# Kernel tuning notes

Hardware: AMD Instinct MI355X
Metric: run time of the kernel (lower is better)

## Reference

```python
import jax, jax.numpy as jnp
import numpy as np

V, C, L, D = 50000, 125000, 500000, 128


def _l2norm(x):
    n = jnp.sqrt(jnp.sum(x * x, axis=-1, keepdims=True))
    return x / jnp.maximum(n, 1e-12)


def _combine(x, W1, b1, W2, b2):
    # SymmetricSumCombine element op: normalize(sigmoid(layer1(x)) + layer2(x));
    # the outer sum over set members is done by segment_sum by the caller.
    return _l2norm(jax.nn.sigmoid(x @ W1 + b1) + (x @ W2 + b2))


def setup_inputs() -> dict:
    key = jax.random.key(0)
    ks = jax.random.split(key, 22)
    s = 1.0 / np.sqrt(D)
    w = lambda k: jax.random.normal(k, (D, D), jnp.float32) * s
    b = lambda k: jax.random.normal(k, (D,), jnp.float32) * s
    return {
        "variables": jax.random.normal(ks[0], (V, D), jnp.float32),
        "lit_var": jax.random.randint(ks[1], (L,), 0, V, jnp.int32),
        "lit_sign": jax.random.randint(ks[2], (L,), 0, 2, jnp.int32),
        "lit_clause": jnp.sort(jax.random.randint(ks[3], (L,), 0, C, jnp.int32)),
        "clause_var": jax.random.randint(ks[4], (C,), 0, V, jnp.int32),
        "neg_W": w(ks[5]), "neg_b": b(ks[6]),
        "vc_W1": w(ks[7]), "vc_b1": b(ks[8]), "vc_W2": w(ks[9]), "vc_b2": b(ks[10]),
        "cc_W1": w(ks[11]), "cc_b1": b(ks[12]), "cc_W2": w(ks[13]), "cc_b2": b(ks[14]),
        "W_z": w(ks[15]), "U_z": w(ks[16]), "W_r": w(ks[17]), "U_r": w(ks[18]),
        "W_h": w(ks[19]), "U_h": w(ks[20]),
    }


def reference(variables, lit_var, lit_sign, lit_clause, clause_var,
              neg_W, neg_b, vc_W1, vc_b1, vc_W2, vc_b2,
              cc_W1, cc_b1, cc_W2, cc_b2,
              W_z, U_z, W_r, U_r, W_h, U_h):
    n_vars = variables.shape[0]
    n_clauses = clause_var.shape[0]
    # gather per-literal variable embeddings, negate negative literals
    v = variables[lit_var]  # [L, D]
    v = jnp.where((lit_sign > 0)[:, None], v @ neg_W + neg_b, v)
    # variable_combiner per literal, summed into clause embeddings
    t = _combine(v, vc_W1, vc_b1, vc_W2, vc_b2)  # [L, D]
    ce = jax.ops.segment_sum(t, lit_clause, num_segments=n_clauses)  # [C, D]
    # clause_combiner per clause, summed into owner variable message
    c = _combine(ce, cc_W1, cc_b1, cc_W2, cc_b2)  # [C, D]
    av = jax.ops.segment_sum(c, clause_var, num_segments=n_vars)  # [V, D]
    # variables with no clauses keep their own embedding as the message
    cnt = jnp.zeros((n_vars,), jnp.float32).at[clause_var].add(1.0)
    av = jnp.where((cnt > 0)[:, None], av, variables)
    # GRU update
    z = jax.nn.sigmoid(av @ W_z + variables @ U_z)
    r = jax.nn.sigmoid(av @ W_r + variables @ U_r)
    h_tilda = jnp.tanh(av @ W_h + (r * variables) @ U_h)
    return (1.0 - z) * variables + z * h_tilda
```

## Files before the change

### kernel.cpp

```cpp
#include <hip/hip_runtime.h>

#define V_N 50000
#define C_N 125000
#define L_N 500000
#define NCH2 31250

typedef __attribute__((ext_vector_type(8))) short short8;
typedef __attribute__((ext_vector_type(4))) float f32x4;

__device__ inline unsigned short f2bf(float f) {
  union { float f; unsigned u; } v; v.f = f;
  unsigned r = v.u + 0x7FFFu + ((v.u >> 16) & 1u);
  return (unsigned short)(r >> 16);
}
__device__ inline float bf2f(unsigned short h) {
  union { unsigned u; float f; } v; v.u = ((unsigned)h) << 16;
  return v.f;
}
__device__ inline float sigm(float x) { return 1.f / (1.f + __expf(-x)); }
__device__ inline unsigned packbf2(float a0, float a1) {
  return (unsigned)f2bf(a0) | ((unsigned)f2bf(a1) << 16);
}

struct WPtrs { const float* w[11]; };

__global__ __launch_bounds__(256) void k_front(
    WPtrs p, unsigned short* __restrict__ wt,
    const int* __restrict__ lit_var, const int* __restrict__ lit_sign,
    const int* __restrict__ lit_clause, int* __restrict__ pmeta,
    int* __restrict__ bnd, const int* __restrict__ clause_var,
    int* __restrict__ cnt, int* __restrict__ dst) {
  int b = blockIdx.x;
  if (b < 704) {
    int idx = b * 256 + threadIdx.x;
    int m = idx >> 14;
    int e14 = idx & 16383;
    int chunk = e14 >> 9;
    int rem = e14 & 511;
    int kq = rem >> 7;
    int lan15 = (rem >> 3) & 15;
    int e = rem & 7;
    int col = ((chunk >> 3) << 5) + (((chunk >> 2) & 1) << 4) + lan15;
    int k = ((chunk & 3) << 5) + (kq << 3) + e;
    wt[idx] = f2bf(p.w[m][k * 128 + col]);
  } else if (b < 2658) {
    int i = (b - 704) * 256 + threadIdx.x;
    if (i < L_N)
      pmeta[i] = lit_var[i] | (lit_sign[i] << 16) | ((lit_clause[i] & 63) << 17);
  } else if (b < 2781) {
    int i = (b - 2658) * 256 + threadIdx.x;
    if (i <= NCH2) {
      int key = i * 4;
      int lo = 0, hi = L_N;
      while (lo < hi) {
        int mid = (lo + hi) >> 1;
        if (lit_clause[mid] < key) lo = mid + 1; else hi = mid;
      }
      bnd[i] = lo;
    }
  } else {
    int i = (b - 2781) * 256 + threadIdx.x;
    if (i < C_N) {
      int v = clause_var[i];
      dst[i] = atomicAdd(&cnt[v], 1);
    }
  }
}

__device__ inline void load_bfrags(const unsigned short* __restrict__ Wt,
                                   short8 B[2][4], int wave, int lane) {
#pragma unroll
  for (int ct = 0; ct < 2; ++ct)
#pragma unroll
    for (int ks = 0; ks < 4; ++ks)
      B[ct][ks] = *(const short8*)(Wt + (((wave << 3) + (ct << 2) + ks) << 9) +
                                   (lane << 3));
}

__device__ inline void gemm_reg(const unsigned short (*__restrict__ xs)[136],
                                const short8 B[2][4], f32x4 acc[4][2], int lane) {
  const int lan15 = lane & 15, kq = lane >> 4;
#pragma unroll
  for (int ks = 0; ks < 4; ++ks) {
#pragma unroll
    for (int rt = 0; rt < 4; ++rt) {
      short8 a = *(const short8*)(&xs[rt * 16 + lan15][ks * 32 + kq * 8]);
#pragma unroll
      for (int ct = 0; ct < 2; ++ct)
        acc[rt][ct] = __builtin_amdgcn_mfma_f32_16x16x32_bf16(a, B[ct][ks], acc[rt][ct], 0, 0, 0);
    }
  }
}

__device__ inline void zero_acc(f32x4 acc[4][2]) {
#pragma unroll
  for (int rt = 0; rt < 4; ++rt)
#pragma unroll
    for (int ct = 0; ct < 2; ++ct) acc[rt][ct] = (f32x4)(0.f);
}

__device__ inline void gemm_reg32(const unsigned short (*__restrict__ xs)[136],
                                  const short8 B[2][4], f32x4 acc[2][2], int lane) {
  const int lan15 = lane & 15, kq = lane >> 4;
#pragma unroll
  for (int ks = 0; ks < 4; ++ks) {
#pragma unroll
    for (int rt = 0; rt < 2; ++rt) {
      short8 a = *(const short8*)(&xs[rt * 16 + lan15][ks * 32 + kq * 8]);
#pragma unroll
      for (int ct = 0; ct < 2; ++ct)
        acc[rt][ct] = __builtin_amdgcn_mfma_f32_16x16x32_bf16(a, B[ct][ks], acc[rt][ct], 0, 0, 0);
    }
  }
}

__device__ inline void zero_acc2(f32x4 acc[2][2]) {
#pragma unroll
  for (int rt = 0; rt < 2; ++rt)
#pragma unroll
    for (int ct = 0; ct < 2; ++ct) acc[rt][ct] = (f32x4)(0.f);
}

__device__ inline void stage_f32_32(const float* __restrict__ base, long vb, int nrows,
                                    unsigned short (*__restrict__ dst)[136], int tid) {
  int r = tid >> 3, cq = (tid & 7) * 16;
  long v = vb + r;
  bool valid = v < nrows;
  const float* src = valid ? base + v * 128 : base;
#pragma unroll
  for (int j = 0; j < 16; j += 4) {
    float4 x4 = *(const float4*)(src + cq + j);
    if (!valid) { x4.x = 0.f; x4.y = 0.f; x4.z = 0.f; x4.w = 0.f; }
    dst[r][cq + j + 0] = f2bf(x4.x);
    dst[r][cq + j + 1] = f2bf(x4.y);
    dst[r][cq + j + 2] = f2bf(x4.z);
    dst[r][cq + j + 3] = f2bf(x4.w);
  }
}

__global__ __launch_bounds__(256, 2) void k_tables(
    const float* __restrict__ vars,
    const unsigned short* __restrict__ negWt, const float* __restrict__ negb,
    const unsigned short* __restrict__ W1t, const float* __restrict__ b1,
    const unsigned short* __restrict__ W2t, const float* __restrict__ b2,
    unsigned short* __restrict__ t_pos, unsigned short* __restrict__ t_neg) {
  __shared__ unsigned short xs[32][136];
  __shared__ unsigned short ys[32][136];
  __shared__ float ssp[32][4];
  const int tid = threadIdx.x;
  const int wave = tid >> 6, lane = tid & 63;
  const int lan15 = lane & 15, kq = lane >> 4;
  const long vb = (long)blockIdx.x * 32;

  stage_f32_32(vars, vb, V_N, xs, tid);
  __syncthreads();

  float nb[2], bb1[2], bb2[2];
#pragma unroll
  for (int ct = 0; ct < 2; ++ct) {
    int col = wave * 32 + ct * 16 + lan15;
    nb[ct] = negb[col]; bb1[ct] = b1[col]; bb2[ct] = b2[col];
  }
  {
    short8 BN[2][4];
    load_bfrags(negWt, BN, wave, lane);
    f32x4 acc[2][2];
    zero_acc2(acc);
    gemm_reg32(xs, BN, acc, lane);
#pragma unroll
    for (int rt = 0; rt < 2; ++rt)
#pragma unroll
      for (int ct = 0; ct < 2; ++ct) {
        int col = wave * 32 + ct * 16 + lan15;
#pragma unroll
        for (int reg = 0; reg < 4; ++reg)
          ys[rt * 16 + kq * 4 + reg][col] = f2bf(acc[rt][ct][reg] + nb[ct]);
      }
  }
  __syncthreads();

  short8 B1f[2][4], B2f[2][4];
  load_bfrags(W1t, B1f, wave, lane);
  load_bfrags(W2t, B2f, wave, lane);

#pragma unroll
  for (int pass = 0; pass < 2; ++pass) {
    const unsigned short (*A)[136] = pass ? ys : xs;
    unsigned short* dst = pass ? t_neg : t_pos;
    f32x4 a1[2][2], a2[2][2];
    zero_acc2(a1); zero_acc2(a2);
    gemm_reg32(A, B1f, a1, lane);
    gemm_reg32(A, B2f, a2, lane);
    float s[2][2][4]; float ss[2][4];
#pragma unroll
    for (int rt = 0; rt < 2; ++rt) {
#pragma unroll
      for (int reg = 0; reg < 4; ++reg) ss[rt][reg] = 0.f;
#pragma unroll
      for (int ct = 0; ct < 2; ++ct)
#pragma unroll
        for (int reg = 0; reg < 4; ++reg) {
          float v = sigm(a1[rt][ct][reg] + bb1[ct]) + (a2[rt][ct][reg] + bb2[ct]);
          s[rt][ct][reg] = v; ss[rt][reg] += v * v;
        }
    }
#pragma unroll
    for (int rt = 0; rt < 2; ++rt)
#pragma unroll
      for (int reg = 0; reg < 4; ++reg) {
        float v = ss[rt][reg];
        v += __shfl_xor(v, 1); v += __shfl_xor(v, 2);
        v += __shfl_xor(v, 4); v += __shfl_xor(v, 8);
        if (lan15 == 0) ssp[rt * 16 + kq * 4 + reg][wave] = v;
      }
    __syncthreads();
#pragma unroll
    for (int rt = 0; rt < 2; ++rt)
#pragma unroll
      for (int reg = 0; reg < 4; ++reg) {
        int row = rt * 16 + kq * 4 + reg;
        float tot = ssp[row][0] + ssp[row][1] + ssp[row][2] + ssp[row][3];
        float inv = 1.f / fmaxf(sqrtf(tot), 1e-12f);
        long vr = vb + row;
        if (vr < V_N) {
#pragma unroll
          for (int ct = 0; ct < 2; ++ct)
            dst[vr * 128 + wave * 32 + ct * 16 + lan15] = f2bf(s[rt][ct][reg] * inv);
        }
      }
    __syncthreads();
  }
}

__global__ __launch_bounds__(256) void k_scan_pre(const int* __restrict__ cnt,
                                                  int* __restrict__ bsum) {
  __shared__ int sh[256];
  const int tid = threadIdx.x;
  int i = blockIdx.x * 256 + tid;
  int v = (i < V_N) ? cnt[i] : 0;
  sh[tid] = v;
  __syncthreads();
  for (int off = 1; off < 256; off <<= 1) {
    int add = (tid >= off) ? sh[tid - off] : 0;
    __syncthreads();
    sh[tid] += add;
    __syncthreads();
  }
  if (tid == 255) bsum[blockIdx.x] = sh[255];
}

__global__ __launch_bounds__(256) void k_scan_mid(int* __restrict__ bsum, int nb) {
  __shared__ int sh[256];
  const int tid = threadIdx.x;
  int v = (tid < nb) ? bsum[tid] : 0;
  sh[tid] = v;
  __syncthreads();
  for (int off = 1; off < 256; off <<= 1) {
    int add = (tid >= off) ? sh[tid - off] : 0;
    __syncthreads();
    sh[tid] += add;
    __syncthreads();
  }
  if (tid < nb) bsum[tid] = sh[tid] - v;
}

__global__ __launch_bounds__(256) void k_scan_post(const int* __restrict__ cnt,
                                                   const int* __restrict__ bsum,
                                                   int* __restrict__ col_start) {
  __shared__ int sh[256];
  const int tid = threadIdx.x;
  int i = blockIdx.x * 256 + tid;
  int v = (i < V_N) ? cnt[i] : 0;
  sh[tid] = v;
  __syncthreads();
  for (int off = 1; off < 256; off <<= 1) {
    int add = (tid >= off) ? sh[tid - off] : 0;
    __syncthreads();
    sh[tid] += add;
    __syncthreads();
  }
  if (i < V_N) col_start[i + 1] = sh[tid] + bsum[blockIdx.x];
  if (i == 0) col_start[0] = 0;
}

__global__ __launch_bounds__(256, 4) void k_sc_clause(
    const int* __restrict__ pmeta, const int* __restrict__ bnd,
    const unsigned short* __restrict__ t_pos,
    const unsigned short* __restrict__ t_neg,
    const int* __restrict__ dst, const int* __restrict__ col_start,
    const int* __restrict__ clause_var,
    const unsigned short* __restrict__ W1t, const float* __restrict__ b1,
    const unsigned short* __restrict__ W2t, const float* __restrict__ b2,
    unsigned short* __restrict__ crows) {
  __shared__ unsigned short xs[64][136];
  __shared__ float ssp[64][4];
  __shared__ int dsts[64];
  const int tid = threadIdx.x;
  const int wave = tid >> 6, lane = tid & 63;
  const int lan15 = lane & 15, kq = lane >> 4;
  const int cb = blockIdx.x * 64;

  {
    int r = tid >> 2, cq = (tid & 3) * 32;
    uint4 z = make_uint4(0, 0, 0, 0);
    *(uint4*)&xs[r][cq + 0] = z;
    *(uint4*)&xs[r][cq + 8] = z;
    *(uint4*)&xs[r][cq + 16] = z;
    *(uint4*)&xs[r][cq + 24] = z;
  }
  if (tid < 64) {
    int c = cb + tid;
    dsts[tid] = (c < C_N) ? dst[c] + col_start[clause_var[c]] : -1;
  }
  {
    const int li = lane & 15;
    const int qbase = lane & 48;
    const int c8 = li * 8;
    int ci = blockIdx.x * 16 + (wave << 2) + kq;
    int i0 = ci < NCH2 ? ci : NCH2;
    int i1 = (ci + 1) < NCH2 ? (ci + 1) : NCH2;
    int ws = bnd[i0], we = bnd[i1];
    float s0 = 0.f, s1 = 0.f, s2 = 0.f, s3 = 0.f;
    float s4 = 0.f, s5 = 0.f, s6 = 0.f, s7 = 0.f;
    int cur = -1;
    for (int r = ws; r < we; r += 16) {
      int idx = r + li;
      int m = (idx < we) ? pmeta[idx] : 0;
      int n = we - r; if (n > 16) n = 16;
#pragma unroll
      for (int h = 0; h < 2; ++h) {
        int nn = n - h * 8;
        if (nn > 8) nn = 8;
        if (nn > 0) {
          int mj[8]; uint4 u[8];
#pragma unroll
          for (int j = 0; j < 8; ++j) {
            int mm = __shfl(m, qbase + h * 8 + j);
            mj[j] = mm;
            int v = mm & 0xFFFF;
            const unsigned short* tb = (mm & 0x10000) ? t_neg : t_pos;
            u[j] = *(const uint4*)(tb + (long)v * 128 + c8);
          }
#pragma unroll
          for (int j = 0; j < 8; ++j) {
            if (j < nn) {
              int rc = mj[j] >> 17;
              if (rc != cur) {
                if (cur >= 0) {
                  uint4 pk;
                  pk.x = packbf2(s0, s1); pk.y = packbf2(s2, s3);
                  pk.z = packbf2(s4, s5); pk.w = packbf2(s6, s7);
                  *(uint4*)&xs[cur][c8] = pk;
                }
                cur = rc;
                s0 = s1 = s2 = s3 = s4 = s5 = s6 = s7 = 0.f;
              }
              s0 += bf2f((unsigned short)u[j].x);
              s1 += bf2f((unsigned short)(u[j].x >> 16));
              s2 += bf2f((unsigned short)u[j].y);
              s3 += bf2f((unsigned short)(u[j].y >> 16));
              s4 += bf2f((unsigned short)u[j].z);
              s5 += bf2f((unsigned short)(u[j].z >> 16));
              s6 += bf2f((unsigned short)u[j].w);
              s7 += bf2f((unsigned short)(u[j].w >> 16));
            }
          }
        }
      }
    }
    if (cur >= 0) {
      uint4 pk;
      pk.x = packbf2(s0, s1); pk.y = packbf2(s2, s3);
      pk.z = packbf2(s4, s5); pk.w = packbf2(s6, s7);
      *(uint4*)&xs[cur][c8] = pk;
    }
  }
  __syncthreads();

  short8 B1f[2][4], B2f[2][4];
  load_bfrags(W1t, B1f, wave, lane);
  load_bfrags(W2t, B2f, wave, lane);
  float bb1[2], bb2[2];
#pragma unroll
  for (int ct = 0; ct < 2; ++ct) {
    int col = wave * 32 + ct * 16 + lan15;
    bb1[ct] = b1[col]; bb2[ct] = b2[col];
  }
  f32x4 a1[4][2], a2[4][2];
  zero_acc(a1); zero_acc(a2);
  gemm_reg(xs, B1f, a1, lane);
  gemm_reg(xs, B2f, a2, lane);
  float s[4][2][4]; float ss[4][4];
#pragma unroll
  for (int rt = 0; rt < 4; ++rt) {
#pragma unroll
    for (int reg = 0; reg < 4; ++reg) ss[rt][reg] = 0.f;
#pragma unroll
    for (int ct = 0; ct < 2; ++ct)
#pragma unroll
      for (int reg = 0; reg < 4; ++reg) {
        float v = sigm(a1[rt][ct][reg] + bb1[ct]) + (a2[rt][ct][reg] + bb2[ct]);
        s[rt][ct][reg] = v; ss[rt][reg] += v * v;
      }
  }
#pragma unroll
  for (int rt = 0; rt < 4; ++rt)
#pragma unroll
    for (int reg = 0; reg < 4; ++reg) {
      float v = ss[rt][reg];
      v += __shfl_xor(v, 1); v += __shfl_xor(v, 2);
      v += __shfl_xor(v, 4); v += __shfl_xor(v, 8);
      if (lan15 == 0) ssp[rt * 16 + kq * 4 + reg][wave] = v;
    }
  __syncthreads();
#pragma unroll
  for (int rt = 0; rt < 4; ++rt)
#pragma unroll
    for (int reg = 0; reg < 4; ++reg) {
      int row = rt * 16 + kq * 4 + reg;
      float tot = ssp[row][0] + ssp[row][1] + ssp[row][2] + ssp[row][3];
      float inv = 1.f / fmaxf(sqrtf(tot), 1e-12f);
      int dd = dsts[row];
      if (dd >= 0) {
#pragma unroll
        for (int ct = 0; ct < 2; ++ct)
          crows[(long)dd * 128 + wave * 32 + ct * 16 + lan15] =
              f2bf(s[rt][ct][reg] * inv);
      }
    }
}

__global__ __launch_bounds__(256, 2) void k_gru(
    const float* __restrict__ vars,
    const unsigned short* __restrict__ crows, const int* __restrict__ col_start,
    const unsigned short* __restrict__ Wzt, const unsigned short* __restrict__ Uzt,
    const unsigned short* __restrict__ Wrt, const unsigned short* __restrict__ Urt,
    const unsigned short* __restrict__ Wht, const unsigned short* __restrict__ Uht,
    float* __restrict__ out) {
  __shared__ unsigned short as_[32][136];
  __shared__ unsigned short vs[32][136];
  const int tid = threadIdx.x;
  const int wave = tid >> 6, lane = tid & 63;
  const int lan15 = lane & 15, kq = lane >> 4;
  const long vb = (long)blockIdx.x * 32;

  {
    int r = tid >> 3, cq = (tid & 7) * 16;
    long v = vb + r;
    if (v < V_N) {
      int s0 = col_start[v], s1 = col_start[v + 1];
      if (s1 > s0) {
        float acc[16];
#pragma unroll
        for (int j = 0; j < 16; ++j) acc[j] = 0.f;
        for (int t = s0; t < s1; ++t) {
          const unsigned short* rp = crows + (long)t * 128 + cq;
#pragma unroll
          for (int j = 0; j < 16; j += 8) {
            short8 u = *(const short8*)(rp + j);
#pragma unroll
            for (int e = 0; e < 8; ++e) acc[j + e] += bf2f((unsigned short)u[e]);
          }
        }
#pragma unroll
        for (int j = 0; j < 16; ++j) as_[r][cq + j] = f2bf(acc[j]);
      } else {
#pragma unroll
        for (int j = 0; j < 16; j += 4) {
          float4 x4 = *(const float4*)(vars + v * 128 + cq + j);
          as_[r][cq + j + 0] = f2bf(x4.x);
          as_[r][cq + j + 1] = f2bf(x4.y);
          as_[r][cq + j + 2] = f2bf(x4.z);
          as_[r][cq + j + 3] = f2bf(x4.w);
        }
      }
    } else {
#pragma unroll
      for (int j = 0; j < 16; ++j) as_[r][cq + j] = 0;
    }
  }
  stage_f32_32(vars, vb, V_N, vs, tid);
  __syncthreads();

  f32x4 az[2][2];
  zero_acc2(az);
  {
    short8 BA[2][4], BB[2][4];
    load_bfrags(Wzt, BA, wave, lane);
    load_bfrags(Uzt, BB, wave, lane);
    gemm_reg32(as_, BA, az, lane);
    gemm_reg32(vs, BB, az, lane);
  }
  f32x4 ar[2][2];
  zero_acc2(ar);
  {
    short8 BA[2][4], BB[2][4];
    load_bfrags(Wrt, BA, wave, lane);
    load_bfrags(Urt, BB, wave, lane);
    gemm_reg32(as_, BA, ar, lane);
    gemm_reg32(vs, BB, ar, lane);
  }
  __syncthreads();
#pragma unroll
  for (int rt = 0; rt < 2; ++rt)
#pragma unroll
    for (int ct = 0; ct < 2; ++ct) {
      int col = wave * 32 + ct * 16 + lan15;
#pragma unroll
      for (int reg = 0; reg < 4; ++reg) {
        int row = rt * 16 + kq * 4 + reg;
        float rr = sigm(ar[rt][ct][reg]);
        float vf = bf2f(vs[row][col]);
        vs[row][col] = f2bf(rr * vf);
      }
    }
  __syncthreads();
  f32x4 ah[2][2];
  zero_acc2(ah);
  {
    short8 BA[2][4], BB[2][4];
    load_bfrags(Wht, BA, wave, lane);
    load_bfrags(Uht, BB, wave, lane);
    gemm_reg32(as_, BA, ah, lane);
    gemm_reg32(vs, BB, ah, lane);
  }
#pragma unroll
  for (int rt = 0; rt < 2; ++rt)
#pragma unroll
    for (int ct = 0; ct < 2; ++ct) {
      int col = wave * 32 + ct * 16 + lan15;
#pragma unroll
      for (int reg = 0; reg < 4; ++reg) {
        int row = rt * 16 + kq * 4 + reg;
        long v = vb + row;
        if (v < V_N) {
          float z = sigm(az[rt][ct][reg]);
          float h = tanhf(ah[rt][ct][reg]);
          float vf = vars[v * 128 + col];
          out[v * 128 + col] = (1.f - z) * vf + z * h;
        }
      }
    }
}

extern "C" void kernel_launch(void* const* d_in, const int* in_sizes, int n_in,
                              void* d_out, int out_size, void* d_ws, size_t ws_size,
                              hipStream_t stream) {
  const float* vars = (const float*)d_in[0];
  const int* lit_var = (const int*)d_in[1];
  const int* lit_sign = (const int*)d_in[2];
  const int* lit_clause = (const int*)d_in[3];
  const int* clause_var = (const int*)d_in[4];
  const float* negW = (const float*)d_in[5];
  const float* negb = (const float*)d_in[6];
  const float* vcW1 = (const float*)d_in[7];
  const float* vcb1 = (const float*)d_in[8];
  const float* vcW2 = (const float*)d_in[9];
  const float* vcb2 = (const float*)d_in[10];
  const float* ccW1 = (const float*)d_in[11];
  const float* ccb1 = (const float*)d_in[12];
  const float* ccW2 = (const float*)d_in[13];
  const float* ccb2 = (const float*)d_in[14];
  const float* Wz = (const float*)d_in[15];
  const float* Uz = (const float*)d_in[16];
  const float* Wr = (const float*)d_in[17];
  const float* Ur = (const float*)d_in[18];
  const float* Wh = (const float*)d_in[19];
  const float* Uh = (const float*)d_in[20];

  unsigned char* ws = (unsigned char*)d_ws;
  unsigned short* wt = (unsigned short*)ws;
  unsigned short* t_pos = (unsigned short*)(ws + 360448);
  unsigned short* t_neg = (unsigned short*)(ws + 13160448);
  unsigned short* crows = (unsigned short*)(ws + 25960448);
  int* col_start = (int*)(ws + 58000000);
  int* cnt = (int*)(ws + 58300000);
  int* dst = (int*)(ws + 58600000);
  int* bsum = (int*)(ws + 59200000);
  int* bnd = (int*)(ws + 59300000);
  int* pmeta = (int*)(ws + 59500000);
  if (ws_size < (size_t)61500000) return;

  const int NB = (V_N + 255) / 256;

  WPtrs p;
  p.w[0] = negW; p.w[1] = vcW1; p.w[2] = vcW2; p.w[3] = ccW1; p.w[4] = ccW2;
  p.w[5] = Wz; p.w[6] = Uz; p.w[7] = Wr; p.w[8] = Ur; p.w[9] = Wh; p.w[10] = Uh;

  hipMemsetAsync(ws + 58300000, 0, (size_t)200000, stream);
  hipLaunchKernelGGL(k_front, dim3(3270), dim3(256), 0, stream, p, wt,
                     lit_var, lit_sign, lit_clause, pmeta, bnd, clause_var,
                     cnt, dst);

  hipLaunchKernelGGL(k_scan_pre, dim3(NB), dim3(256), 0, stream, cnt, bsum);
  hipLaunchKernelGGL(k_scan_mid, dim3(1), dim3(256), 0, stream, bsum, NB);
  hipLaunchKernelGGL(k_scan_post, dim3(NB), dim3(256), 0, stream, cnt, bsum, col_start);

  hipLaunchKernelGGL(k_tables, dim3((V_N + 31) / 32), dim3(256), 0, stream,
                     vars, wt + 0, negb, wt + 16384, vcb1, wt + 2 * 16384, vcb2,
                     t_pos, t_neg);

  hipLaunchKernelGGL(k_sc_clause, dim3((C_N + 63) / 64), dim3(256), 0, stream,
                     pmeta, bnd, t_pos, t_neg, dst, col_start, clause_var,
                     wt + 3 * 16384, ccb1, wt + 4 * 16384, ccb2, crows);

  hipLaunchKernelGGL(k_gru, dim3((V_N + 31) / 32), dim3(256), 0, stream,
                     vars, crows, col_start,
                     wt + 5 * 16384, wt + 6 * 16384, wt + 7 * 16384,
                     wt + 8 * 16384, wt + 9 * 16384, wt + 10 * 16384,
                     (float*)d_out);
}
```

Baseline: 145.2 us.

## Compute clause segment sums via MFMA one-hot matmul instead of scalar accumulation

The per-clause segment sum of literal rows is now computed as a matrix product. A one-hot selection matrix, built from the clause indices in pmeta, is multiplied with gathered bf16 literal rows using 16x16x32 bf16 MFMA, and each wave covers 16 clause rows over 32-literal batches. This replaces the serial branchy run-length accumulation and the shared-memory zeroing, and the result is written directly into xs. In exchange, the gathers become scalar 16-bit loads strided by 16 instead of uint4 loads, and MFMA work is spent on mostly zero entries.

```diff
diff --git a/kernel.cpp b/kernel.cpp
--- a/kernel.cpp
+++ b/kernel.cpp
@@ -18,9 +18,6 @@
   return v.f;
 }
 __device__ inline float sigm(float x) { return 1.f / (1.f + __expf(-x)); }
-__device__ inline unsigned packbf2(float a0, float a1) {
-  return (unsigned)f2bf(a0) | ((unsigned)f2bf(a1) << 16);
-}
 
 struct WPtrs { const float* w[11]; };
 
@@ -300,81 +297,64 @@
   const int lan15 = lane & 15, kq = lane >> 4;
   const int cb = blockIdx.x * 64;
 
-  {
-    int r = tid >> 2, cq = (tid & 3) * 32;
-    uint4 z = make_uint4(0, 0, 0, 0);
-    *(uint4*)&xs[r][cq + 0] = z;
-    *(uint4*)&xs[r][cq + 8] = z;
-    *(uint4*)&xs[r][cq + 16] = z;
-    *(uint4*)&xs[r][cq + 24] = z;
-  }
   if (tid < 64) {
     int c = cb + tid;
     dsts[tid] = (c < C_N) ? dst[c] + col_start[clause_var[c]] : -1;
   }
-  {
-    const int li = lane & 15;
-    const int qbase = lane & 48;
-    const int c8 = li * 8;
-    int ci = blockIdx.x * 16 + (wave << 2) + kq;
-    int i0 = ci < NCH2 ? ci : NCH2;
-    int i1 = (ci + 1) < NCH2 ? (ci + 1) : NCH2;
-    int ws = bnd[i0], we = bnd[i1];
-    float s0 = 0.f, s1 = 0.f, s2 = 0.f, s3 = 0.f;
-    float s4 = 0.f, s5 = 0.f, s6 = 0.f, s7 = 0.f;
-    int cur = -1;
-    for (int r = ws; r < we; r += 16) {
-      int idx = r + li;
-      int m = (idx < we) ? pmeta[idx] : 0;
-      int n = we - r; if (n > 16) n = 16;
-#pragma unroll
-      for (int h = 0; h < 2; ++h) {
-        int nn = n - h * 8;
-        if (nn > 8) nn = 8;
-        if (nn > 0) {
-          int mj[8]; uint4 u[8];
-#pragma unroll
-          for (int j = 0; j < 8; ++j) {
-            int mm = __shfl(m, qbase + h * 8 + j);
-            mj[j] = mm;
-            int v = mm & 0xFFFF;
-            const unsigned short* tb = (mm & 0x10000) ? t_neg : t_pos;
-            u[j] = *(const uint4*)(tb + (long)v * 128 + c8);
-          }
-#pragma unroll
-          for (int j = 0; j < 8; ++j) {
-            if (j < nn) {
-              int rc = mj[j] >> 17;
-              if (rc != cur) {
-                if (cur >= 0) {
-                  uint4 pk;
-                  pk.x = packbf2(s0, s1); pk.y = packbf2(s2, s3);
-                  pk.z = packbf2(s4, s5); pk.w = packbf2(s6, s7);
-                  *(uint4*)&xs[cur][c8] = pk;
-                }
-                cur = rc;
-                s0 = s1 = s2 = s3 = s4 = s5 = s6 = s7 = 0.f;
-              }
-              s0 += bf2f((unsigned short)u[j].x);
-              s1 += bf2f((unsigned short)(u[j].x >> 16));
-              s2 += bf2f((unsigned short)u[j].y);
-              s3 += bf2f((unsigned short)(u[j].y >> 16));
-              s4 += bf2f((unsigned short)u[j].z);
-              s5 += bf2f((unsigned short)(u[j].z >> 16));
-              s6 += bf2f((unsigned short)u[j].w);
-              s7 += bf2f((unsigned short)(u[j].w >> 16));
-            }
-          }
-        }
-      }
-    }
-    if (cur >= 0) {
-      uint4 pk;
-      pk.x = packbf2(s0, s1); pk.y = packbf2(s2, s3);
-      pk.z = packbf2(s4, s5); pk.w = packbf2(s6, s7);
-      *(uint4*)&xs[cur][c8] = pk;
-    }
-  }
+
+  int bi0 = blockIdx.x * 16 + wave * 4;
+  int i0 = bi0 < NCH2 ? bi0 : NCH2;
+  int i1 = (bi0 + 4) < NCH2 ? (bi0 + 4) : NCH2;
+  int ws = bnd[i0], we = bnd[i1];
+
+  f32x4 acc[8];
+#pragma unroll
+  for (int s = 0; s < 8; ++s) acc[s] = (f32x4)(0.f);
+
+  const int mtarget = wave * 16 + lan15;
+
+  for (int base = ws; base < we; base += 32) {
+    int mm = 0x00FE0000;
+    if (lane < 32) {
+      int idx = base + lane;
+      if (idx < we) mm = pmeta[idx];
+    }
+    unsigned au[4];
+#pragma unroll
+    for (int pp = 0; pp < 4; ++pp) {
+      int m0 = __shfl(mm, 8 * kq + 2 * pp);
+      int m1 = __shfl(mm, 8 * kq + 2 * pp + 1);
+      unsigned lo = (((m0 >> 17) & 127) == mtarget) ? 0x3F80u : 0u;
+      unsigned hi = (((m1 >> 17) & 127) == mtarget) ? 0x3F800000u : 0u;
+      au[pp] = lo | hi;
+    }
+    unsigned t16[8][8];
+#pragma unroll
+    for (int e = 0; e < 8; ++e) {
+      int mv = __shfl(mm, 8 * kq + e);
+      int v = mv & 0xFFFF;
+      const unsigned short* rp =
+          ((mv & 0x10000) ? t_neg : t_pos) + (long)v * 128 + lan15;
+#pragma unroll
+      for (int s = 0; s < 8; ++s) t16[e][s] = rp[s * 16];
+    }
+    union { unsigned u[4]; short8 s8; } ua;
+    ua.u[0] = au[0]; ua.u[1] = au[1]; ua.u[2] = au[2]; ua.u[3] = au[3];
+#pragma unroll
+    for (int s = 0; s < 8; ++s) {
+      union { unsigned u[4]; short8 s8; } ub;
+#pragma unroll
+      for (int d = 0; d < 4; ++d)
+        ub.u[d] = t16[2 * d][s] | (t16[2 * d + 1][s] << 16);
+      acc[s] = __builtin_amdgcn_mfma_f32_16x16x32_bf16(ua.s8, ub.s8, acc[s], 0, 0, 0);
+    }
+  }
+
+#pragma unroll
+  for (int s = 0; s < 8; ++s)
+#pragma unroll
+    for (int reg = 0; reg < 4; ++reg)
+      xs[wave * 16 + 4 * kq + reg][s * 16 + lan15] = f2bf(acc[s][reg]);
   __syncthreads();
 
   short8 B1f[2][4], B2f[2][4];
```

After: 142.3 us. 1.02x faster.
